# Kernel optimization log

Hardware: AMD Instinct MI355X
Metric: run time of the kernel (lower is better)

## Reference

```python
import jax, jax.numpy as jnp
import numpy as np

B, N, E, H = 4, 1024, 1024, 16
D = E // H

def setup_inputs() -> dict:
    key = jax.random.key(0)
    ks = jax.random.split(key, 5)
    return {
        "x": jax.random.normal(ks[0], (B, N, E), dtype=jnp.float32),
        "Wqkv": jax.random.normal(ks[1], (E, 3 * E), dtype=jnp.float32) * 0.02,
        "bqkv": jax.random.normal(ks[2], (3 * E,), dtype=jnp.float32) * 0.02,
        "Wfc": jax.random.normal(ks[3], (E, E), dtype=jnp.float32) * 0.02,
        "bfc": jax.random.normal(ks[4], (E,), dtype=jnp.float32) * 0.02,
    }

def reference(x, Wqkv, bqkv, Wfc, bfc):
    b, n, e = x.shape
    h, d = H, E // H
    qkv = x @ Wqkv + bqkv                      # [b, n, 3e]
    q, k, v = jnp.split(qkv, 3, axis=-1)       # each [b, n, e]
    # view to [b, n, h, d] then RAW reshape to [b, h, n, d] (faithful to original,
    # which uses .reshape, not transpose — mixes seq/head axes)
    q = q.reshape(b, n, h, d).reshape(b, h, n, d)
    k = k.reshape(b, n, h, d).reshape(b, h, n, d)
    v = v.reshape(b, n, h, d).reshape(b, h, n, d)
    scores = jnp.einsum('bhqd,bhkd->bhqk', q, k) / jnp.sqrt(jnp.float32(d))
    causal = jnp.triu(jnp.ones((n, n), dtype=bool), k=1)  # True above diagonal
    scores = jnp.where(causal, -jnp.inf, scores)
    attn = jax.nn.softmax(scores, axis=-1)
    out = jnp.einsum('bhqk,bhkd->bhqd', attn, v)          # [b, h, n, d]
    # raw reshape back to [b, n, h, d] then flatten heads (faithful)
    out = out.reshape(b, n, h, d).reshape(b, n, e)
    return out @ Wfc + bfc
```

## Files before the change

kernel.cpp:

```cpp
#include <hip/hip_runtime.h>


typedef __bf16 bf16x8 __attribute__((ext_vector_type(8)));
typedef float f32x4 __attribute__((ext_vector_type(4)));

#define QSCALE 0.18033688011112042f
#define DEFER_THR 11.0f

__device__ __forceinline__ unsigned short f2bf(float f) {
    unsigned u = __float_as_uint(f);
    u += 0x7fffu + ((u >> 16) & 1u);
    return (unsigned short)(u >> 16);
}

__device__ __forceinline__ unsigned cvtpk_bf16(float lo, float hi) {
    unsigned r;
    asm("v_cvt_pk_bf16_f32 %0, %1, %2" : "=v"(r) : "v"(lo), "v"(hi));
    return r;
}

union FragU { uint4 u; bf16x8 v; };

__device__ __forceinline__ bf16x8 ld_frag(const unsigned short* p) {
    FragU x; x.u = *(const uint4*)p; return x.v;
}

__device__ __forceinline__ void gload_lds16(const void* g, void* l) {
    __builtin_amdgcn_global_load_lds(
        (const __attribute__((address_space(1))) void*)g,
        (__attribute__((address_space(3))) void*)l, 16, 0, 0);
}

__global__ __launch_bounds__(256) void prep(
    const float* __restrict__ x,    unsigned short* __restrict__ xb,
    const float* __restrict__ Wqkv, unsigned short* __restrict__ wqkvT,
    const float* __restrict__ Wfc,  unsigned short* __restrict__ wfcT)
{
    __shared__ float tile[32][33];
    int bid = blockIdx.x;
    int tx = threadIdx.x & 31, ty = threadIdx.x >> 5;
    if (bid < 3072) {
        int c0 = (bid % 96) * 32, r0 = (bid / 96) * 32;
        for (int i = ty; i < 32; i += 8)
            tile[i][tx] = Wqkv[(r0 + i) * 3072 + c0 + tx];
        __syncthreads();
        for (int i = ty; i < 32; i += 8)
            wqkvT[(long)(c0 + i) * 1024 + r0 + tx] = f2bf(tile[tx][i]);
    } else if (bid < 4096) {
        int b2 = bid - 3072;
        int c0 = (b2 % 32) * 32, r0 = (b2 / 32) * 32;
        for (int i = ty; i < 32; i += 8)
            tile[i][tx] = Wfc[(r0 + i) * 1024 + c0 + tx];
        __syncthreads();
        for (int i = ty; i < 32; i += 8)
            wfcT[(long)(c0 + i) * 1024 + r0 + tx] = f2bf(tile[tx][i]);
    } else {
        const int n4 = 1 << 20;
        for (int i = (bid - 4096) * 256 + threadIdx.x; i < n4; i += 1024 * 256) {
            float4 f = ((const float4*)x)[i];
            unsigned a = (unsigned)f2bf(f.x) | ((unsigned)f2bf(f.y) << 16);
            unsigned b = (unsigned)f2bf(f.z) | ((unsigned)f2bf(f.w) << 16);
            ((uint2*)xb)[i] = make_uint2(a, b);
        }
    }
}

__global__ void transpose_v(const unsigned short* __restrict__ v,
                            unsigned short* __restrict__ vt) {
    __shared__ unsigned short tile[32][33];
    int bh = blockIdx.z;
    int n0 = blockIdx.x * 32, d0 = blockIdx.y * 32;
    const unsigned short* src = v + (long)bh * 65536;
    unsigned short* dst = vt + (long)bh * 65536;
    for (int i = threadIdx.y; i < 32; i += 8)
        tile[i][threadIdx.x] = src[(n0 + i) * 64 + d0 + threadIdx.x];
    __syncthreads();
    for (int i = threadIdx.y; i < 32; i += 8)
        dst[(d0 + i) * 1024 + n0 + threadIdx.x] = tile[threadIdx.x][i];
}

template <int MODE>
__global__ __launch_bounds__(256) void gemm128(
    const unsigned short* __restrict__ A,
    const unsigned short* __restrict__ Bt,
    const float* __restrict__ bias,
    unsigned short* __restrict__ qb,
    unsigned short* __restrict__ kb,
    unsigned short* __restrict__ vb,
    float* __restrict__ outf)
{
    const int K = 1024;
    __shared__ unsigned short As[2][4096];
    __shared__ unsigned short Bs[2][4096];
    int t = threadIdx.x, lane = t & 63, w = t >> 6;
    int wm = w >> 1, wn = w & 1;
    int lrow = lane >> 4, lcol = lane & 15;

    const int NX  = (MODE == 0) ? 24 : 8;
    const int CPX = (MODE == 0) ? 96 : 32;
    int id = blockIdx.x;
    int idp = (id & 7) * CPX + (id >> 3);
    int tn0 = (idp % NX) * 128, tm0 = (idp / NX) * 128;

    int seg0 = w * 1024;
    int seg1 = (w + 4) * 1024;
    int off0 = seg0 + lane * 16, off1 = seg1 + lane * 16;
    int r0 = off0 >> 6, cb0 = off0 & 63;
    int r1 = off1 >> 6, cb1 = off1 & 63;

    const char* gA = (const char*)A;
    const char* gB = (const char*)Bt;

    f32x4 acc[4][4] = {};

    auto STAGE = [&](int buf, int kt) {
        long kby = (long)kt * 2;
        gload_lds16(gA + (long)(tm0 + r0) * 2048 + kby + cb0, (char*)&As[buf][0] + seg0);
        gload_lds16(gA + (long)(tm0 + r1) * 2048 + kby + cb1, (char*)&As[buf][0] + seg1);
        gload_lds16(gB + (long)(tn0 + r0) * 2048 + kby + cb0, (char*)&Bs[buf][0] + seg0);
        gload_lds16(gB + (long)(tn0 + r1) * 2048 + kby + cb1, (char*)&Bs[buf][0] + seg1);
    };

    STAGE(0, 0);
    asm volatile("s_waitcnt vmcnt(0)");
    __syncthreads();

    int cur = 0;
    for (int kt = 0; kt < K; kt += 32) {
        if (kt + 32 < K) STAGE(cur ^ 1, kt + 32);

        bf16x8 af[4], bfr[4];
        #pragma unroll
        for (int mi = 0; mi < 4; ++mi)
            af[mi] = ld_frag(&As[cur][0] + (wm * 64 + mi * 16 + lcol) * 32 + lrow * 8);
        #pragma unroll
        for (int ni = 0; ni < 4; ++ni)
            bfr[ni] = ld_frag(&Bs[cur][0] + (wn * 64 + ni * 16 + lcol) * 32 + lrow * 8);
        #pragma unroll
        for (int mi = 0; mi < 4; ++mi)
            #pragma unroll
            for (int ni = 0; ni < 4; ++ni)
                acc[mi][ni] = __builtin_amdgcn_mfma_f32_16x16x32_bf16(af[mi], bfr[ni], acc[mi][ni], 0, 0, 0);

        __syncthreads();
        cur ^= 1;
    }

    #pragma unroll
    for (int mi = 0; mi < 4; ++mi) {
        int gr0 = tm0 + wm * 64 + mi * 16 + lrow * 4;
        #pragma unroll
        for (int ni = 0; ni < 4; ++ni) {
            int gc = tn0 + wn * 64 + ni * 16 + lcol;
            float bv = bias[gc];
            if (MODE == 0) {
                int sec = gc >> 10, ei = gc & 1023;
                unsigned short* dst = sec == 0 ? qb : (sec == 1 ? kb : vb);
                if (sec == 0) {
                    #pragma unroll
                    for (int r = 0; r < 4; ++r)
                        dst[(long)(gr0 + r) * 1024 + ei] = f2bf((acc[mi][ni][r] + bv) * QSCALE);
                } else {
                    #pragma unroll
                    for (int r = 0; r < 4; ++r)
                        dst[(long)(gr0 + r) * 1024 + ei] = f2bf(acc[mi][ni][r] + bv);
                }
            } else {
                #pragma unroll
                for (int r = 0; r < 4; ++r)
                    outf[(long)(gr0 + r) * 1024 + gc] = acc[mi][ni][r] + bv;
            }
        }
    }
}

__global__ __launch_bounds__(256) void attn(
    const unsigned short* __restrict__ qbuf,
    const unsigned short* __restrict__ kbuf,
    const unsigned short* __restrict__ vtbuf,
    unsigned short* __restrict__ obuf)
{
    __shared__ unsigned short Ks[2][4096];
    __shared__ unsigned short Vs[2][4096];
    __shared__ unsigned short Ps[4][32][40];

    int id = blockIdx.x;
    int xcd = id & 7, s_ = id >> 3;
    int j  = 7 - (s_ >> 3);
    int bh = xcd + 8 * (s_ & 7);

    const char* Kb = (const char*)(kbuf + (long)bh * 65536);
    const char* Vb = (const char*)(vtbuf + (long)bh * 65536);
    const unsigned short* Q = qbuf + (long)bh * 65536;
    unsigned short* O = obuf + (long)bh * 65536;

    int t = threadIdx.x, lane = t & 63, w = t >> 6;
    int lrow = lane >> 4, lcol = lane & 15;
    const float NEG = -__builtin_inff();

    int qbase = j * 128 + w * 32;
    int T = 2 * j + 2;

    int row0 = w * 8 + (lane >> 3);
    int slot = (((lane & 7) ^ (lane >> 3)) << 4);

    auto STAGE = [&](int buf, int kt) {
        long k2 = (long)kt * 2;
        gload_lds16(Kb + (k2 + row0 * 2) * 64 + slot,        (char*)&Ks[buf][0] + w * 1024);
        gload_lds16(Kb + (k2 + (row0 + 32) * 2) * 64 + slot, (char*)&Ks[buf][0] + 4096 + w * 1024);
        gload_lds16(Vb + (long)row0 * 2048 + k2 + slot,        (char*)&Vs[buf][0] + w * 1024);
        gload_lds16(Vb + (long)(row0 + 32) * 2048 + k2 + slot, (char*)&Vs[buf][0] + 4096 + w * 1024);
    };

    bf16x8 qf[2][2];
    #pragma unroll
    for (int qg = 0; qg < 2; ++qg)
        #pragma unroll
        for (int kc = 0; kc < 2; ++kc)
            qf[qg][kc] = ld_frag(Q + (long)(qbase + qg * 16 + lcol) * 64 + kc * 32 + lrow * 8);

    f32x4 acc[2][4] = {};
    float m_i[2] = {NEG, NEG};
    float lsum[2][2] = {{0.f, 0.f}, {0.f, 0.f}};

    STAGE(0, 0);
    STAGE(1, 64);

    for (int tt = 0; tt < T; ++tt) {
        if (tt + 1 < T) asm volatile("s_waitcnt vmcnt(4)" ::: "memory");
        else            asm volatile("s_waitcnt vmcnt(0)" ::: "memory");
        __builtin_amdgcn_s_barrier();

        int cur = tt & 1;
        #pragma unroll
        for (int ks = 0; ks < 2; ++ks) {
            int kt_sub = tt * 64 + ks * 32;
            if (kt_sub <= qbase) {
                bf16x8 kf[2][2], vf[4];
                #pragma unroll
                for (int kg = 0; kg < 2; ++kg)
                    #pragma unroll
                    for (int kc = 0; kc < 2; ++kc) {
                        int row = ks * 32 + kg * 16 + lcol;
                        kf[kg][kc] = ld_frag(&Ks[cur][row * 64 + (((kc * 4 + lrow) ^ (row & 7)) << 3)]);
                    }
                #pragma unroll
                for (int dg = 0; dg < 4; ++dg) {
                    int row = dg * 16 + lcol;
                    vf[dg] = ld_frag(&Vs[cur][row * 64 + (((ks * 4 + lrow) ^ (row & 7)) << 3)]);
                }

                f32x4 s[2][2] = {};
                __builtin_amdgcn_s_setprio(1);
                #pragma unroll
                for (int kg = 0; kg < 2; ++kg)
                    #pragma unroll
                    for (int kc = 0; kc < 2; ++kc) {
                        s[0][kg] = __builtin_amdgcn_mfma_f32_16x16x32_bf16(kf[kg][kc], qf[0][kc], s[0][kg], 0, 0, 0);
                        s[1][kg] = __builtin_amdgcn_mfma_f32_16x16x32_bf16(kf[kg][kc], qf[1][kc], s[1][kg], 0, 0, 0);
                    }
                __builtin_amdgcn_s_setprio(0);

                bool diag = (kt_sub == qbase);
                if (diag) {
                    #pragma unroll
                    for (int qg = 0; qg < 2; ++qg)
                        #pragma unroll
                        for (int kg = 0; kg < 2; ++kg)
                            #pragma unroll
                            for (int r = 0; r < 4; ++r)
                                if (kg * 16 + lrow * 4 + r > qg * 16 + lcol)
                                    s[qg][kg][r] = NEG;
                }
                float lmax[2];
                #pragma unroll
                for (int qg = 0; qg < 2; ++qg) {
                    float a0 = fmaxf(s[qg][0][0], s[qg][0][1]), a1 = fmaxf(s[qg][0][2], s[qg][0][3]);
                    float a2 = fmaxf(s[qg][1][0], s[qg][1][1]), a3 = fmaxf(s[qg][1][2], s[qg][1][3]);
                    lmax[qg] = fmaxf(fmaxf(a0, a1), fmaxf(a2, a3));
                }
                bool ok = (lmax[0] <= m_i[0] + DEFER_THR) && (lmax[1] <= m_i[1] + DEFER_THR);
                if (!__all(ok)) {
                    #pragma unroll
                    for (int qg = 0; qg < 2; ++qg) {
                        float mx = fmaxf(lmax[qg], __shfl_xor(lmax[qg], 16));
                        mx = fmaxf(mx, __shfl_xor(mx, 32));
                        float mnew = fmaxf(m_i[qg], mx);
                        float alpha = exp2f(m_i[qg] - mnew);
                        m_i[qg] = mnew;
                        lsum[qg][0] *= alpha;
                        lsum[qg][1] *= alpha;
                        #pragma unroll
                        for (int dg = 0; dg < 4; ++dg)
                            #pragma unroll
                            for (int r = 0; r < 4; ++r)
                                acc[qg][dg][r] *= alpha;
                    }
                }
                #pragma unroll
                for (int qg = 0; qg < 2; ++qg) {
                    float p[8];
                    #pragma unroll
                    for (int kg = 0; kg < 2; ++kg)
                        #pragma unroll
                        for (int r = 0; r < 4; ++r)
                            p[kg * 4 + r] = exp2f(s[qg][kg][r] - m_i[qg]);
                    lsum[qg][0] += (p[0] + p[1]) + (p[2] + p[3]);
                    lsum[qg][1] += (p[4] + p[5]) + (p[6] + p[7]);
                    unsigned u0 = cvtpk_bf16(p[0], p[1]);
                    unsigned u1 = cvtpk_bf16(p[2], p[3]);
                    unsigned u2 = cvtpk_bf16(p[4], p[5]);
                    unsigned u3 = cvtpk_bf16(p[6], p[7]);
                    *(uint2*)&Ps[w][qg * 16 + lcol][lrow * 4]      = make_uint2(u0, u1);
                    *(uint2*)&Ps[w][qg * 16 + lcol][16 + lrow * 4] = make_uint2(u2, u3);
                }

                bf16x8 pb[2];
                pb[0] = ld_frag(&Ps[w][lcol][lrow * 8]);
                pb[1] = ld_frag(&Ps[w][16 + lcol][lrow * 8]);

                __builtin_amdgcn_s_setprio(1);
                #pragma unroll
                for (int dg = 0; dg < 4; ++dg) {
                    acc[0][dg] = __builtin_amdgcn_mfma_f32_16x16x32_bf16(vf[dg], pb[0], acc[0][dg], 0, 0, 0);
                    acc[1][dg] = __builtin_amdgcn_mfma_f32_16x16x32_bf16(vf[dg], pb[1], acc[1][dg], 0, 0, 0);
                }
                __builtin_amdgcn_s_setprio(0);
            }
        }

        __builtin_amdgcn_s_barrier();
        if (tt + 2 < T) STAGE(cur, (tt + 2) * 64);
    }

    #pragma unroll
    for (int qg = 0; qg < 2; ++qg) {
        float lr = lsum[qg][0] + lsum[qg][1];
        lr += __shfl_xor(lr, 16);
        lr += __shfl_xor(lr, 32);
        float inv = 1.f / lr;
        int q = qbase + qg * 16 + lcol;
        #pragma unroll
        for (int dg = 0; dg < 4; ++dg) {
            ushort4 pk;
            pk.x = f2bf(acc[qg][dg][0] * inv);
            pk.y = f2bf(acc[qg][dg][1] * inv);
            pk.z = f2bf(acc[qg][dg][2] * inv);
            pk.w = f2bf(acc[qg][dg][3] * inv);
            *(ushort4*)&O[(long)q * 64 + dg * 16 + lrow * 4] = pk;
        }
    }
}

extern "C" void kernel_launch(void* const* d_in, const int* in_sizes, int n_in,
                              void* d_out, int out_size, void* d_ws, size_t ws_size,
                              hipStream_t stream) {
    const float* x    = (const float*)d_in[0];
    const float* Wqkv = (const float*)d_in[1];
    const float* bqkv = (const float*)d_in[2];
    const float* Wfc  = (const float*)d_in[3];
    const float* bfc  = (const float*)d_in[4];
    float* out = (float*)d_out;

    unsigned short* ws    = (unsigned short*)d_ws;
    unsigned short* xb    = ws;
    unsigned short* wqkvT = xb + (4u << 20);
    unsigned short* wfcT  = wqkvT + (3u << 20);
    unsigned short* qb    = wfcT + (1u << 20);
    unsigned short* kb    = qb + (4u << 20);
    unsigned short* vb    = kb + (4u << 20);
    unsigned short* vbT   = xb;
    unsigned short* ob    = vb;

    prep<<<dim3(5120), dim3(256), 0, stream>>>(x, xb, Wqkv, wqkvT, Wfc, wfcT);
    gemm128<0><<<dim3(768), dim3(256), 0, stream>>>(xb, wqkvT, bqkv, qb, kb, vb, nullptr);
    transpose_v<<<dim3(32, 2, 64), dim3(32, 8), 0, stream>>>(vb, vbT);
    attn<<<dim3(512), dim3(256), 0, stream>>>(qb, kb, vbT, ob);
    gemm128<1><<<dim3(256), dim3(256), 0, stream>>>(ob, wfcT, bfc, nullptr, nullptr, nullptr, out);
}
```

Measured before the change: 111.4 us.

## Swizzle GEMM LDS tiles and deepen async prefetch with partial vmcnt waits

The GEMM kernel now XOR-swizzles the 16-byte chunk each thread loads from global memory into LDS, and fragment reads use the matching swizzled offsets, to cut LDS bank conflicts on the ds_read path. The main loop is also restructured: two stages are issued up front, each iteration waits only for the older batch with vmcnt(4) plus a raw s_barrier, and the next-next stage is issued after compute. This aims to keep global loads in flight across compute instead of draining every iteration. It relies on exact vmcnt accounting and on raw barriers without LDS waitcnt, which is fragile.

Result: no change. 112.6 us (+1.1%).

```diff
diff --git a/kernel.cpp b/kernel.cpp
--- a/kernel.cpp
+++ b/kernel.cpp
@@ -89,7 +89,6 @@
     unsigned short* __restrict__ vb,
     float* __restrict__ outf)
 {
-    const int K = 1024;
     __shared__ unsigned short As[2][4096];
     __shared__ unsigned short Bs[2][4096];
     int t = threadIdx.x, lane = t & 63, w = t >> 6;
@@ -105,45 +104,56 @@
     int seg0 = w * 1024;
     int seg1 = (w + 4) * 1024;
     int off0 = seg0 + lane * 16, off1 = seg1 + lane * 16;
-    int r0 = off0 >> 6, cb0 = off0 & 63;
-    int r1 = off1 >> 6, cb1 = off1 & 63;
+    int r0 = off0 >> 6, g0 = ((((off0 >> 4) & 3) ^ ((r0 >> 1) & 3)) << 4);
+    int r1 = off1 >> 6, g1 = ((((off1 >> 4) & 3) ^ ((r1 >> 1) & 3)) << 4);
 
     const char* gA = (const char*)A;
     const char* gB = (const char*)Bt;
 
+    int aoff[4], boff[4];
+    #pragma unroll
+    for (int mi = 0; mi < 4; ++mi) {
+        int row = wm * 64 + mi * 16 + lcol;
+        aoff[mi] = row * 32 + ((lrow ^ ((row >> 1) & 3)) << 3);
+    }
+    #pragma unroll
+    for (int ni = 0; ni < 4; ++ni) {
+        int row = wn * 64 + ni * 16 + lcol;
+        boff[ni] = row * 32 + ((lrow ^ ((row >> 1) & 3)) << 3);
+    }
+
     f32x4 acc[4][4] = {};
 
     auto STAGE = [&](int buf, int kt) {
         long kby = (long)kt * 2;
-        gload_lds16(gA + (long)(tm0 + r0) * 2048 + kby + cb0, (char*)&As[buf][0] + seg0);
-        gload_lds16(gA + (long)(tm0 + r1) * 2048 + kby + cb1, (char*)&As[buf][0] + seg1);
-        gload_lds16(gB + (long)(tn0 + r0) * 2048 + kby + cb0, (char*)&Bs[buf][0] + seg0);
-        gload_lds16(gB + (long)(tn0 + r1) * 2048 + kby + cb1, (char*)&Bs[buf][0] + seg1);
+        gload_lds16(gA + (long)(tm0 + r0) * 2048 + kby + g0, (char*)&As[buf][0] + seg0);
+        gload_lds16(gA + (long)(tm0 + r1) * 2048 + kby + g1, (char*)&As[buf][0] + seg1);
+        gload_lds16(gB + (long)(tn0 + r0) * 2048 + kby + g0, (char*)&Bs[buf][0] + seg0);
+        gload_lds16(gB + (long)(tn0 + r1) * 2048 + kby + g1, (char*)&Bs[buf][0] + seg1);
     };
 
     STAGE(0, 0);
-    asm volatile("s_waitcnt vmcnt(0)");
-    __syncthreads();
-
-    int cur = 0;
-    for (int kt = 0; kt < K; kt += 32) {
-        if (kt + 32 < K) STAGE(cur ^ 1, kt + 32);
-
+    STAGE(1, 32);
+
+    for (int tt = 0; tt < 32; ++tt) {
+        if (tt < 31) asm volatile("s_waitcnt vmcnt(4)" ::: "memory");
+        else         asm volatile("s_waitcnt vmcnt(0)" ::: "memory");
+        __builtin_amdgcn_s_barrier();
+
+        int cur = tt & 1;
         bf16x8 af[4], bfr[4];
         #pragma unroll
-        for (int mi = 0; mi < 4; ++mi)
-            af[mi] = ld_frag(&As[cur][0] + (wm * 64 + mi * 16 + lcol) * 32 + lrow * 8);
-        #pragma unroll
-        for (int ni = 0; ni < 4; ++ni)
-            bfr[ni] = ld_frag(&Bs[cur][0] + (wn * 64 + ni * 16 + lcol) * 32 + lrow * 8);
+        for (int mi = 0; mi < 4; ++mi) af[mi] = ld_frag(&As[cur][aoff[mi]]);
+        #pragma unroll
+        for (int ni = 0; ni < 4; ++ni) bfr[ni] = ld_frag(&Bs[cur][boff[ni]]);
         #pragma unroll
         for (int mi = 0; mi < 4; ++mi)
             #pragma unroll
             for (int ni = 0; ni < 4; ++ni)
                 acc[mi][ni] = __builtin_amdgcn_mfma_f32_16x16x32_bf16(af[mi], bfr[ni], acc[mi][ni], 0, 0, 0);
 
-        __syncthreads();
-        cur ^= 1;
+        __builtin_amdgcn_s_barrier();
+        if (tt + 2 < 32) STAGE(cur, (tt + 2) * 32);
     }
 
     #pragma unroll
```
